# Kernel optimization log

Hardware: AMD Instinct MI355X
Metric: run time of the kernel (lower is better)

## Reference

```python
import jax, jax.numpy as jnp
import numpy as np

B, N, K = 8, 8192, 8192   # batch, out_features, in_features
PACK = 8
# maybe_pack_idxs places original column offset POS[b] into nibble b
POS = [0, 2, 4, 6, 1, 3, 5, 7]
# inverse permutation: original offset p comes from nibble INV[p]
INV = jnp.array([0, 4, 1, 5, 2, 6, 3, 7], dtype=jnp.int32)


def setup_inputs() -> dict:
    key = jax.random.key(0)
    k1, k2 = jax.random.split(key)
    x = jax.random.normal(k1, (B, K), dtype=jnp.float32)
    # random 4-bit codebook indices, then pack exactly like maybe_pack_idxs
    idxs = jax.random.randint(k2, (N, K), 0, 16, dtype=jnp.int32)
    g = idxs.reshape(N, K // PACK, PACK)
    packed = jnp.zeros((N, K // PACK), dtype=jnp.int32)
    for b, p in enumerate(POS):
        packed = packed + (g[..., p] << jnp.int32(4 * b))
    return {"input": x, "Qidxs": packed}


def decompress_weight(Qidxs):
    # Qidxs: [N, K/8] int32 -> W: [N, K] float32
    shifts = (jnp.arange(PACK, dtype=jnp.int32) * 4)
    nibbles = (Qidxs[..., None] >> shifts) & 0xF       # [N, K/8, 8], nibble order
    unpacked = nibbles[..., INV]                        # restore original column order
    # grid = arange(-8, 8) + 0.5  =>  value = idx - 7.5
    return unpacked.reshape(N, K).astype(jnp.float32) - 7.5


def reference(input, Qidxs):
    W = decompress_weight(Qidxs)          # [N, K]
    return input @ W.T                    # [B, N]
```

## Files before the change

### kernel.cpp

```cpp
#include <hip/hip_runtime.h>
#include <hip/hip_fp16.h>
#include <stdint.h>


typedef _Float16 half8 __attribute__((ext_vector_type(8)));
typedef float floatx4 __attribute__((ext_vector_type(4)));

union H2U { unsigned u; __half2 h; };
union V4H8 { uint4 u4; half8 h8; };

__device__ __forceinline__ unsigned unpack_even(unsigned w, __half2 c1, __half2 c2) {
    H2U t; t.u = (w & 0x000F000Fu) | 0x64006400u;
    t.h = __hadd2(__hadd2(t.h, c1), c2);
    return t.u;
}
__device__ __forceinline__ unsigned unpack_odd(unsigned w, __half2 cs, __half2 cc) {
    H2U t; t.u = (w & 0x00F000F0u) | 0x64006400u;
    t.h = __hfma2(t.h, cs, cc);
    return t.u;
}

#define TPITCH 528
#define TBYTES (256 * TPITCH)
#define BP     528
#define BWAVE  (16 * BP)
#define NWV    8
#define REDOFF (NWV * BWAVE)
#define LDS_BYTES (REDOFF + NWV * 128 * 4)

__global__ void build_atable(const float* __restrict__ x, char* __restrict__ tbl)
{
    const int S = blockIdx.x;
    const int t = threadIdx.x;
    if (t > 32) return;
    uint4 v = make_uint4(0u, 0u, 0u, 0u);
    if (t < 32) {
        const int u = t >> 3, r = t & 7;
        const float4* x4 = (const float4*)x;
        float4 fa = x4[r * 2048 + 8 * S + 2 * u];
        float4 fb = x4[r * 2048 + 8 * S + 2 * u + 1];
        H2U a0, a1, a2, a3;
        a0.h = __floats2half2_rn(fa.x, fa.y);
        a1.h = __floats2half2_rn(fa.z, fa.w);
        a2.h = __floats2half2_rn(fb.x, fb.y);
        a3.h = __floats2half2_rn(fb.z, fb.w);
        v = make_uint4(a0.u, a1.u, a2.u, a3.u);
    }
    const int slot = (t < 32) ? ((t >> 3) * 8 + (t & 7)) : 32;
    *(uint4*)(tbl + S * TPITCH + slot * 16) = v;
}

__global__ __launch_bounds__(512, 4)
void hi4b_gemm(const char* __restrict__ atbl, const int* __restrict__ q,
               float* __restrict__ out)
{
    extern __shared__ char lds[];
    const int tid  = threadIdx.x;
    const int lane = tid & 63;
    const int wv   = tid >> 6;
    const int n0   = blockIdx.x * 16;

    const int r16 = lane & 15;
    const int u4  = lane >> 4;

    {
        const int r0 = lane >> 2, ci = lane & 3;
        const uint4* q4 = (const uint4*)q;
        const int gb = (n0 + r0) * 256 + wv * 32 + ci;
        char* Bw = lds + wv * BWAVE + r0 * BP + ci * 16;
        uint4 v[8];
        #pragma unroll
        for (int i = 0; i < 8; ++i) v[i] = q4[gb + 4 * i];
        #pragma unroll
        for (int i = 0; i < 8; ++i) *(uint4*)(Bw + i * 64) = v[i];
    }

    const int  slot = (r16 < 8) ? (u4 * 8 + r16) : 32;
    const char* ap  = atbl + (wv * 32) * TPITCH + slot * 16;

    uint4 T0[4], T1[4];
    auto refill = [&](uint4 (&T)[4], int t) {
        const char* p = ap + t * (4 * TPITCH);
        #pragma unroll
        for (int i = 0; i < 4; ++i)
            T[i] = *(const uint4*)(p + i * TPITCH);
    };
    refill(T0, 0);
    refill(T1, 1);

    const __half2 c1 = __floats2half2_rn(-1024.0f, -1024.0f);
    const __half2 c2 = __floats2half2_rn(-7.5f, -7.5f);
    const __half2 cs = __floats2half2_rn(0.0625f, 0.0625f);
    const __half2 cc = __floats2half2_rn(-71.5f, -71.5f);

    floatx4 acc = {0.0f, 0.0f, 0.0f, 0.0f};
    const char* bp = lds + wv * BWAVE + r16 * BP + u4 * 4;

    auto comp4 = [&](uint4 (&T)[4], int t) {
        #pragma unroll
        for (int i = 0; i < 4; ++i) {
            unsigned w = *(const unsigned*)(bp + (4 * t + i) * 16);
            unsigned w8 = w >> 8;
            V4H8 Bf;
            Bf.u4.x = unpack_even(w,  c1, c2);
            Bf.u4.y = unpack_odd (w,  cs, cc);
            Bf.u4.z = unpack_even(w8, c1, c2);
            Bf.u4.w = unpack_odd (w8, cs, cc);
            V4H8 A;  A.u4 = T[i];
            acc = __builtin_amdgcn_mfma_f32_16x16x32_f16(A.h8, Bf.h8, acc, 0, 0, 0);
        }
    };

    comp4(T0, 0); refill(T0, 2);
    comp4(T1, 1); refill(T1, 3);
    comp4(T0, 2); refill(T0, 4);
    comp4(T1, 3); refill(T1, 5);
    comp4(T0, 4); refill(T0, 6);
    comp4(T1, 5); refill(T1, 7);
    comp4(T0, 6);
    comp4(T1, 7);

    {
        float* red = (float*)(lds + REDOFF) + wv * 128;
        if (u4 < 2) {
            #pragma unroll
            for (int r = 0; r < 4; ++r)
                red[(u4 * 4 + r) * 16 + r16] = acc[r];
        }
    }
    __syncthreads();
    if (tid < 128) {
        const float* rd = (const float*)(lds + REDOFF);
        float sm = 0.0f;
        #pragma unroll
        for (int w = 0; w < NWV; ++w)
            sm += rd[w * 128 + tid];
        out[(tid >> 4) * 8192 + n0 + (tid & 15)] = sm;
    }
}

extern "C" void kernel_launch(void* const* d_in, const int* in_sizes, int n_in,
                              void* d_out, int out_size, void* d_ws, size_t ws_size,
                              hipStream_t stream)
{
    const float* x = (const float*)d_in[0];
    const int*   q = (const int*)d_in[1];
    float* out = (float*)d_out;
    char*  tbl = (char*)d_ws;

    hipLaunchKernelGGL(build_atable, dim3(256), dim3(64), 0, stream, x, tbl);
    hipLaunchKernelGGL(hi4b_gemm, dim3(512), dim3(512), LDS_BYTES, stream,
                       tbl, q, out);
}
```

Baseline: 17.05 us.

## Load packed weights directly to registers and split K across 16 waves

Drops the LDS staging of packed 4-bit weights. Each lane now loads its 16 weight words straight from global memory into registers, which also changes the slot layout of the activation table to match. The block grows to 1024 threads (16 waves), each covering half the K range it did before, and the cross-wave LDS reduction is widened to match. This removes the LDS store/load round trip and shortens each wave's serial MFMA chain, at the cost of strided, less coalesced global loads, higher register pressure under launch_bounds(1024,4), and more waves in the final reduction.

```diff
diff --git a/kernel.cpp b/kernel.cpp
--- a/kernel.cpp
+++ b/kernel.cpp
@@ -21,12 +21,8 @@
 }
 
 #define TPITCH 528
-#define TBYTES (256 * TPITCH)
-#define BP     528
-#define BWAVE  (16 * BP)
-#define NWV    8
-#define REDOFF (NWV * BWAVE)
-#define LDS_BYTES (REDOFF + NWV * 128 * 4)
+#define NWV    16
+#define LDS_BYTES (NWV * 128 * 4)
 
 __global__ void build_atable(const float* __restrict__ x, char* __restrict__ tbl)
 {
@@ -46,11 +42,11 @@
         a3.h = __floats2half2_rn(fb.z, fb.w);
         v = make_uint4(a0.u, a1.u, a2.u, a3.u);
     }
-    const int slot = (t < 32) ? ((t >> 3) * 8 + (t & 7)) : 32;
+    const int slot = (t < 32) ? t : 32;
     *(uint4*)(tbl + S * TPITCH + slot * 16) = v;
 }
 
-__global__ __launch_bounds__(512, 4)
+__global__ __launch_bounds__(1024, 4)
 void hi4b_gemm(const char* __restrict__ atbl, const int* __restrict__ q,
                float* __restrict__ out)
 {
@@ -63,20 +59,15 @@
     const int r16 = lane & 15;
     const int u4  = lane >> 4;
 
-    {
-        const int r0 = lane >> 2, ci = lane & 3;
-        const uint4* q4 = (const uint4*)q;
-        const int gb = (n0 + r0) * 256 + wv * 32 + ci;
-        char* Bw = lds + wv * BWAVE + r0 * BP + ci * 16;
-        uint4 v[8];
-        #pragma unroll
-        for (int i = 0; i < 8; ++i) v[i] = q4[gb + 4 * i];
-        #pragma unroll
-        for (int i = 0; i < 8; ++i) *(uint4*)(Bw + i * 64) = v[i];
-    }
+    const unsigned* qw = (const unsigned*)q + (size_t)(n0 + r16) * 1024
+                       + wv * 64 + u4;
+    unsigned w[16];
+    #pragma unroll
+    for (int s = 0; s < 16; ++s)
+        w[s] = qw[4 * s];
 
     const int  slot = (r16 < 8) ? (u4 * 8 + r16) : 32;
-    const char* ap  = atbl + (wv * 32) * TPITCH + slot * 16;
+    const char* ap  = atbl + (size_t)(wv * 16) * TPITCH + slot * 16;
 
     uint4 T0[4], T1[4];
     auto refill = [&](uint4 (&T)[4], int t) {
@@ -94,16 +85,15 @@
     const __half2 cc = __floats2half2_rn(-71.5f, -71.5f);
 
     floatx4 acc = {0.0f, 0.0f, 0.0f, 0.0f};
-    const char* bp = lds + wv * BWAVE + r16 * BP + u4 * 4;
 
     auto comp4 = [&](uint4 (&T)[4], int t) {
         #pragma unroll
         for (int i = 0; i < 4; ++i) {
-            unsigned w = *(const unsigned*)(bp + (4 * t + i) * 16);
-            unsigned w8 = w >> 8;
+            unsigned ww = w[4 * t + i];
+            unsigned w8 = ww >> 8;
             V4H8 Bf;
-            Bf.u4.x = unpack_even(w,  c1, c2);
-            Bf.u4.y = unpack_odd (w,  cs, cc);
+            Bf.u4.x = unpack_even(ww, c1, c2);
+            Bf.u4.y = unpack_odd (ww, cs, cc);
             Bf.u4.z = unpack_even(w8, c1, c2);
             Bf.u4.w = unpack_odd (w8, cs, cc);
             V4H8 A;  A.u4 = T[i];
@@ -113,15 +103,11 @@
 
     comp4(T0, 0); refill(T0, 2);
     comp4(T1, 1); refill(T1, 3);
-    comp4(T0, 2); refill(T0, 4);
-    comp4(T1, 3); refill(T1, 5);
-    comp4(T0, 4); refill(T0, 6);
-    comp4(T1, 5); refill(T1, 7);
-    comp4(T0, 6);
-    comp4(T1, 7);
+    comp4(T0, 2);
+    comp4(T1, 3);
 
     {
-        float* red = (float*)(lds + REDOFF) + wv * 128;
+        float* red = (float*)lds + wv * 128;
         if (u4 < 2) {
             #pragma unroll
             for (int r = 0; r < 4; ++r)
@@ -130,11 +116,11 @@
     }
     __syncthreads();
     if (tid < 128) {
-        const float* rd = (const float*)(lds + REDOFF);
+        const float* rd = (const float*)lds;
         float sm = 0.0f;
         #pragma unroll
-        for (int w = 0; w < NWV; ++w)
-            sm += rd[w * 128 + tid];
+        for (int wi = 0; wi < NWV; ++wi)
+            sm += rd[wi * 128 + tid];
         out[(tid >> 4) * 8192 + n0 + (tid & 15)] = sm;
     }
 }
@@ -149,6 +135,6 @@
     char*  tbl = (char*)d_ws;
 
     hipLaunchKernelGGL(build_atable, dim3(256), dim3(64), 0, stream, x, tbl);
-    hipLaunchKernelGGL(hi4b_gemm, dim3(512), dim3(512), LDS_BYTES, stream,
+    hipLaunchKernelGGL(hi4b_gemm, dim3(512), dim3(1024), LDS_BYTES, stream,
                        tbl, q, out);
 }
```

Measured after the change: 29.32 us. +71.9%, slower.
